# Kernel optimization log

Measured on AMD Instinct MI355X. Metric: run time of the kernel, lower is better.

The kernel has to match this reference:

```python
import jax, jax.numpy as jnp
import numpy as np

N_NODES = 100000
SAMPLES = 16


def setup_inputs() -> dict:
    key = jax.random.key(0)
    ks = jax.random.split(key, 9)
    x = jax.random.normal(ks[0], (N_NODES, 128), dtype=jnp.float32)
    neigh_idx = jax.random.randint(ks[1], (N_NODES, SAMPLES), 0, N_NODES)
    batch = jax.random.randint(ks[2], (8192,), 0, N_NODES)
    W1 = jax.random.normal(ks[3], (256, 128), dtype=jnp.float32) * 0.05
    b1 = jax.random.normal(ks[4], (128,), dtype=jnp.float32) * 0.05
    W2 = jax.random.normal(ks[5], (256, 128), dtype=jnp.float32) * 0.05
    b2 = jax.random.normal(ks[6], (128,), dtype=jnp.float32) * 0.05
    Wout = jax.random.normal(ks[7], (128, 64), dtype=jnp.float32) * 0.05
    bout = jax.random.normal(ks[8], (64,), dtype=jnp.float32) * 0.05
    return {"x": x, "neigh_idx": neigh_idx, "batch": batch,
            "W1": W1, "b1": b1, "W2": W2, "b2": b2,
            "Wout": Wout, "bout": bout}


def _sage_layer(h, neigh_idx, W, b):
    # h: [N, d]; gather sampled neighbors -> [N, S, d]; max-aggregate; concat-linear
    neigh = h[neigh_idx]                     # irregular gather, memory-bound core
    agg = jnp.max(neigh, axis=1)             # MaxAggregation over samples
    feats = jnp.concatenate([h, agg], axis=-1)  # [N, 2d]
    return feats @ W + b


def reference(x, neigh_idx, batch, W1, b1, W2, b2, Wout, bout):
    # layer 1: relu(Linear(concat(x, max_neigh(x))))
    h1 = jax.nn.relu(_sage_layer(x, neigh_idx, W1, b1))
    # layer 2 (== n_layers): Linear output (no relu) fed straight into proj_out
    h2 = _sage_layer(h1, neigh_idx, W2, b2)
    out = h2 @ Wout + bout                   # proj_out (Dropout is eval identity)
    return out[batch]
```

## Files before the change

kernel.cpp:

```cpp
#include <hip/hip_runtime.h>
#include <cmath>
#include <cstdint>

#define N_NODES 100000
#define SAMPLES 16
#define DIM 128
#define NBATCH 8192

#define FSTR 264
#define H2STR 132

typedef _Float16 half8 __attribute__((ext_vector_type(8)));
typedef float floatx4 __attribute__((ext_vector_type(4)));

__device__ __forceinline__ half8 h8max(half8 a, half8 b) {
    half8 r;
#pragma unroll
    for (int i = 0; i < 8; ++i) r[i] = (a[i] > b[i]) ? a[i] : b[i];
    return r;
}

__global__ __launch_bounds__(256) void setup_kernel(
    const float* __restrict__ x,
    const float* __restrict__ W1,
    const float* __restrict__ W2,
    const int* __restrict__ batch,
    const int* __restrict__ nidx,
    int* __restrict__ flags,
    _Float16* __restrict__ xh,
    _Float16* __restrict__ W1sw,
    _Float16* __restrict__ W2sw) {
    const int bid = blockIdx.x;
    if (bid < 6250) {
        const size_t base = ((size_t)bid * 256 + threadIdx.x) * 8;
        const float4* xp = (const float4*)(x + base);
        const float4 a = xp[0], b = xp[1];
        half8 v;
        v[0] = (_Float16)a.x; v[1] = (_Float16)a.y;
        v[2] = (_Float16)a.z; v[3] = (_Float16)a.w;
        v[4] = (_Float16)b.x; v[5] = (_Float16)b.y;
        v[6] = (_Float16)b.z; v[7] = (_Float16)b.w;
        *(half8*)(xh + base) = v;
    } else if (bid < 6282) {
        const int tid = (bid - 6250) * 256 + threadIdx.x;
        const int which = tid >> 12;
        const int r = tid & 4095;
        const int kb = r >> 9, nb = (r >> 6) & 7, lane = r & 63;
        const int q = lane >> 4, c = lane & 15;
        const float* W = which ? W2 : W1;
        _Float16* O = which ? W2sw : W1sw;
        const int k0 = kb * 32 + q * 8;
        const int n = nb * 16 + c;
        half8 v;
#pragma unroll
        for (int j = 0; j < 8; ++j) v[j] = (_Float16)W[(size_t)(k0 + j) * DIM + n];
        *(half8*)(O + (size_t)r * 8) = v;
    } else {
        const int j = (bid - 6282) * 256 + threadIdx.x;
        if (j < NBATCH) {
            const int b = batch[j];
            flags[b] = 1;
            const int* row = nidx + (size_t)b * SAMPLES;
#pragma unroll
            for (int s = 0; s < SAMPLES; ++s) flags[row[s]] = 1;
        }
    }
}

__global__ __launch_bounds__(256, 3) void layer1_kernel(
    const _Float16* __restrict__ xh,
    const int* __restrict__ nidx,
    const _Float16* __restrict__ W1sw,
    const float* __restrict__ b1,
    const int* __restrict__ flags,
    _Float16* __restrict__ h1h) {
    const int wave = threadIdx.x >> 6;
    const int lane = threadIdx.x & 63;
    const int q = lane >> 4;
    const int c = lane & 15;
    const int w0 = blockIdx.x * 64 + wave * 16;

    const int i = w0 + c;
    const bool fi = (i < N_NODES) && (flags[i] == 1);

    half8 sk[4], mk[4];
#pragma unroll
    for (int j = 0; j < 4; ++j)
#pragma unroll
        for (int e = 0; e < 8; ++e) { sk[j][e] = (_Float16)0.f; mk[j][e] = (_Float16)(-60000.f); }

    if (fi) {
        const char* xb = (const char*)xh;
        const int4* ip = (const int4*)(nidx + (size_t)i * SAMPLES);
        const int4 i0 = ip[0], i1 = ip[1], i2 = ip[2], i3 = ip[3];
        const int qb = q * 16;
        const int soff = i * 256 + qb;
        int off[16];
        off[0]  = i0.x * 256 + qb; off[1]  = i0.y * 256 + qb;
        off[2]  = i0.z * 256 + qb; off[3]  = i0.w * 256 + qb;
        off[4]  = i1.x * 256 + qb; off[5]  = i1.y * 256 + qb;
        off[6]  = i1.z * 256 + qb; off[7]  = i1.w * 256 + qb;
        off[8]  = i2.x * 256 + qb; off[9]  = i2.y * 256 + qb;
        off[10] = i2.z * 256 + qb; off[11] = i2.w * 256 + qb;
        off[12] = i3.x * 256 + qb; off[13] = i3.y * 256 + qb;
        off[14] = i3.z * 256 + qb; off[15] = i3.w * 256 + qb;
#pragma unroll
        for (int j = 0; j < 4; ++j) {
            sk[j] = *(const half8*)(xb + soff + j * 64);
            half8 v[16];
#pragma unroll
            for (int s = 0; s < 16; ++s)
                v[s] = *(const half8*)(xb + off[s] + j * 64);
#pragma unroll
            for (int s = 0; s < 8; ++s) v[s] = h8max(v[s], v[s + 8]);
#pragma unroll
            for (int s = 0; s < 4; ++s) v[s] = h8max(v[s], v[s + 4]);
            mk[j] = h8max(h8max(v[0], v[1]), h8max(v[2], v[3]));
        }
    }

    floatx4 acc[8];
#pragma unroll
    for (int nb = 0; nb < 8; ++nb) acc[nb] = (floatx4){0.f, 0.f, 0.f, 0.f};
#pragma unroll
    for (int kb = 0; kb < 8; ++kb) {
        const half8 a = (kb < 4) ? sk[kb] : mk[kb - 4];
#pragma unroll
        for (int nb = 0; nb < 8; ++nb) {
            const half8 b = *(const half8*)(W1sw + (size_t)((kb * 8 + nb) * 64 + lane) * 8);
            acc[nb] = __builtin_amdgcn_mfma_f32_16x16x32_f16(a, b, acc[nb], 0, 0, 0);
        }
    }

#pragma unroll
    for (int r = 0; r < 4; ++r) {
        const int node = w0 + q * 4 + r;
        if (node >= N_NODES || flags[node] != 1) continue;
#pragma unroll
        for (int nb = 0; nb < 8; ++nb) {
            const int n = nb * 16 + c;
            const float v = fmaxf(acc[nb][r] + b1[n], 0.f);
            h1h[(size_t)node * DIM + n] = (_Float16)v;
        }
    }
}

__global__ __launch_bounds__(256) void layer2_kernel(
    const _Float16* __restrict__ h1h,
    const int* __restrict__ nidx,
    const int* __restrict__ batch,
    const _Float16* __restrict__ W2sw,
    const float* __restrict__ b2,
    const float* __restrict__ Wout,
    const float* __restrict__ bout,
    float* __restrict__ out) {
    const int t = threadIdx.x;
    const int wave = t >> 6;
    const int lane = t & 63;
    const int q = lane >> 4, c = lane & 15;
    const int w0 = blockIdx.x * 16;

    __shared__ __align__(16) _Float16 feats[16 * FSTR];
    __shared__ __align__(16) float h2s[16 * H2STR];

    {
        const int m = t >> 4;
        const int cl = t & 15;
        const int node = batch[w0 + m];
        const char* hb = (const char*)h1h;
        const int cb = cl * 16;
        const half8 self = *(const half8*)(hb + node * 256 + cb);
        const int4* ip = (const int4*)(nidx + (size_t)node * SAMPLES);
        const int4 i0 = ip[0], i1 = ip[1], i2 = ip[2], i3 = ip[3];
        int off[16];
        off[0]  = i0.x * 256 + cb; off[1]  = i0.y * 256 + cb;
        off[2]  = i0.z * 256 + cb; off[3]  = i0.w * 256 + cb;
        off[4]  = i1.x * 256 + cb; off[5]  = i1.y * 256 + cb;
        off[6]  = i1.z * 256 + cb; off[7]  = i1.w * 256 + cb;
        off[8]  = i2.x * 256 + cb; off[9]  = i2.y * 256 + cb;
        off[10] = i2.z * 256 + cb; off[11] = i2.w * 256 + cb;
        off[12] = i3.x * 256 + cb; off[13] = i3.y * 256 + cb;
        off[14] = i3.z * 256 + cb; off[15] = i3.w * 256 + cb;
        half8 v[16];
#pragma unroll
        for (int s = 0; s < 16; ++s) v[s] = *(const half8*)(hb + off[s]);
#pragma unroll
        for (int s = 0; s < 8; ++s) v[s] = h8max(v[s], v[s + 8]);
#pragma unroll
        for (int s = 0; s < 4; ++s) v[s] = h8max(v[s], v[s + 4]);
        const half8 mx = h8max(h8max(v[0], v[1]), h8max(v[2], v[3]));
        *(half8*)(feats + m * FSTR + cl * 8) = self;
        *(half8*)(feats + m * FSTR + DIM + cl * 8) = mx;
    }
    __syncthreads();

    const int nb0 = wave * 2;
    floatx4 acc[2];
    acc[0] = (floatx4){0.f, 0.f, 0.f, 0.f};
    acc[1] = (floatx4){0.f, 0.f, 0.f, 0.f};
#pragma unroll
    for (int kb = 0; kb < 8; ++kb) {
        const half8 a = *(const half8*)(feats + c * FSTR + kb * 32 + q * 8);
#pragma unroll
        for (int j = 0; j < 2; ++j) {
            const half8 b = *(const half8*)(W2sw + (size_t)((kb * 8 + nb0 + j) * 64 + lane) * 8);
            acc[j] = __builtin_amdgcn_mfma_f32_16x16x32_f16(a, b, acc[j], 0, 0, 0);
        }
    }
#pragma unroll
    for (int j = 0; j < 2; ++j) {
        const int n = (nb0 + j) * 16 + c;
        const float bias = b2[n];
#pragma unroll
        for (int r = 0; r < 4; ++r)
            h2s[(q * 4 + r) * H2STR + n] = acc[j][r] + bias;
    }
    __syncthreads();

    float accs[4];
    const float bo = bout[lane];
#pragma unroll
    for (int r = 0; r < 4; ++r) accs[r] = bo;
    for (int k4 = 0; k4 < DIM; k4 += 4) {
        float wv[4];
#pragma unroll
        for (int j = 0; j < 4; ++j) wv[j] = Wout[(size_t)(k4 + j) * 64 + lane];
#pragma unroll
        for (int r = 0; r < 4; ++r) {
            const float4 f = *(const float4*)&h2s[(wave * 4 + r) * H2STR + k4];
            accs[r] += f.x * wv[0] + f.y * wv[1] + f.z * wv[2] + f.w * wv[3];
        }
    }
#pragma unroll
    for (int r = 0; r < 4; ++r)
        out[(size_t)(w0 + wave * 4 + r) * 64 + lane] = accs[r];
}

extern "C" void kernel_launch(void* const* d_in, const int* in_sizes, int n_in,
                              void* d_out, int out_size, void* d_ws, size_t ws_size,
                              hipStream_t stream) {
    const float* x    = (const float*)d_in[0];
    const int* nidx   = (const int*)d_in[1];
    const int* batch  = (const int*)d_in[2];
    const float* W1   = (const float*)d_in[3];
    const float* b1   = (const float*)d_in[4];
    const float* W2   = (const float*)d_in[5];
    const float* b2   = (const float*)d_in[6];
    const float* Wout = (const float*)d_in[7];
    const float* bout = (const float*)d_in[8];
    float* out        = (float*)d_out;

    int* flags      = (int*)d_ws;
    _Float16* W1sw  = (_Float16*)((char*)d_ws + 409600);
    _Float16* W2sw  = (_Float16*)((char*)d_ws + 475136);
    _Float16* xh    = (_Float16*)((char*)d_ws + 540672);
    _Float16* h1h   = (_Float16*)((char*)d_ws + 26140672);

    setup_kernel<<<6314, 256, 0, stream>>>(x, W1, W2, batch, nidx, flags, xh, W1sw, W2sw);
    layer1_kernel<<<(N_NODES + 63) / 64, 256, 0, stream>>>(xh, nidx, W1sw, b1, flags, h1h);
    layer2_kernel<<<NBATCH / 16, 256, 0, stream>>>(h1h, nidx, batch, W2sw, b2, Wout, bout, out);
}
```

Baseline: 193.3 us.

## Restructure layer1 to 16 nodes per block with LDS-staged features

Layer1 now handles 16 nodes per block: 16 threads per node each gather one 16-byte chunk from the 16 neighbors, and the self and max features are staged in shared memory. Each wave then computes two of the eight 16-column output tiles with MFMA, reading its A operands from LDS. Per-thread register pressure drops (no eight accumulators and no 4-way unrolled gather), and there are more blocks, so occupancy and memory-level parallelism should rise. The cost is a __syncthreads, extra LDS traffic, and about four times as many blocks, each loading the W1 fragments again.

```diff
diff --git a/kernel.cpp b/kernel.cpp
--- a/kernel.cpp
+++ b/kernel.cpp
@@ -67,79 +67,81 @@
     }
 }
 
-__global__ __launch_bounds__(256, 3) void layer1_kernel(
+__global__ __launch_bounds__(256) void layer1_kernel(
     const _Float16* __restrict__ xh,
     const int* __restrict__ nidx,
     const _Float16* __restrict__ W1sw,
     const float* __restrict__ b1,
     const int* __restrict__ flags,
     _Float16* __restrict__ h1h) {
-    const int wave = threadIdx.x >> 6;
-    const int lane = threadIdx.x & 63;
-    const int q = lane >> 4;
-    const int c = lane & 15;
-    const int w0 = blockIdx.x * 64 + wave * 16;
-
-    const int i = w0 + c;
-    const bool fi = (i < N_NODES) && (flags[i] == 1);
-
-    half8 sk[4], mk[4];
-#pragma unroll
-    for (int j = 0; j < 4; ++j)
-#pragma unroll
-        for (int e = 0; e < 8; ++e) { sk[j][e] = (_Float16)0.f; mk[j][e] = (_Float16)(-60000.f); }
-
+    const int t = threadIdx.x;
+    const int g = t >> 4;
+    const int cl = t & 15;
+    const int i0 = blockIdx.x * 16;
+    const int i = i0 + g;
+
+    __shared__ __align__(16) _Float16 feats[16 * FSTR];
+
+    const bool fi = (flags[i] == 1);
     if (fi) {
         const char* xb = (const char*)xh;
+        const int cb = cl * 16;
+        const half8 self = *(const half8*)(xb + (size_t)i * 256 + cb);
         const int4* ip = (const int4*)(nidx + (size_t)i * SAMPLES);
-        const int4 i0 = ip[0], i1 = ip[1], i2 = ip[2], i3 = ip[3];
-        const int qb = q * 16;
-        const int soff = i * 256 + qb;
+        const int4 a0 = ip[0], a1 = ip[1], a2 = ip[2], a3 = ip[3];
         int off[16];
-        off[0]  = i0.x * 256 + qb; off[1]  = i0.y * 256 + qb;
-        off[2]  = i0.z * 256 + qb; off[3]  = i0.w * 256 + qb;
-        off[4]  = i1.x * 256 + qb; off[5]  = i1.y * 256 + qb;
-        off[6]  = i1.z * 256 + qb; off[7]  = i1.w * 256 + qb;
-        off[8]  = i2.x * 256 + qb; off[9]  = i2.y * 256 + qb;
-        off[10] = i2.z * 256 + qb; off[11] = i2.w * 256 + qb;
-        off[12] = i3.x * 256 + qb; off[13] = i3.y * 256 + qb;
-        off[14] = i3.z * 256 + qb; off[15] = i3.w * 256 + qb;
-#pragma unroll
-        for (int j = 0; j < 4; ++j) {
-            sk[j] = *(const half8*)(xb + soff + j * 64);
-            half8 v[16];
-#pragma unroll
-            for (int s = 0; s < 16; ++s)
-                v[s] = *(const half8*)(xb + off[s] + j * 64);
-#pragma unroll
-            for (int s = 0; s < 8; ++s) v[s] = h8max(v[s], v[s + 8]);
-#pragma unroll
-            for (int s = 0; s < 4; ++s) v[s] = h8max(v[s], v[s + 4]);
-            mk[j] = h8max(h8max(v[0], v[1]), h8max(v[2], v[3]));
-        }
-    }
-
-    floatx4 acc[8];
-#pragma unroll
-    for (int nb = 0; nb < 8; ++nb) acc[nb] = (floatx4){0.f, 0.f, 0.f, 0.f};
+        off[0]  = a0.x * 256 + cb; off[1]  = a0.y * 256 + cb;
+        off[2]  = a0.z * 256 + cb; off[3]  = a0.w * 256 + cb;
+        off[4]  = a1.x * 256 + cb; off[5]  = a1.y * 256 + cb;
+        off[6]  = a1.z * 256 + cb; off[7]  = a1.w * 256 + cb;
+        off[8]  = a2.x * 256 + cb; off[9]  = a2.y * 256 + cb;
+        off[10] = a2.z * 256 + cb; off[11] = a2.w * 256 + cb;
+        off[12] = a3.x * 256 + cb; off[13] = a3.y * 256 + cb;
+        off[14] = a3.z * 256 + cb; off[15] = a3.w * 256 + cb;
+        half8 v[16];
+#pragma unroll
+        for (int s = 0; s < 16; ++s) v[s] = *(const half8*)(xb + off[s]);
+#pragma unroll
+        for (int s = 0; s < 8; ++s) v[s] = h8max(v[s], v[s + 8]);
+#pragma unroll
+        for (int s = 0; s < 4; ++s) v[s] = h8max(v[s], v[s + 4]);
+        const half8 mx = h8max(h8max(v[0], v[1]), h8max(v[2], v[3]));
+        *(half8*)(feats + g * FSTR + cl * 8) = self;
+        *(half8*)(feats + g * FSTR + DIM + cl * 8) = mx;
+    } else {
+        half8 z;
+#pragma unroll
+        for (int e = 0; e < 8; ++e) z[e] = (_Float16)0.f;
+        *(half8*)(feats + g * FSTR + cl * 8) = z;
+        *(half8*)(feats + g * FSTR + DIM + cl * 8) = z;
+    }
+    __syncthreads();
+
+    const int wave = t >> 6;
+    const int lane = t & 63;
+    const int q = lane >> 4, c = lane & 15;
+    const int nb0 = wave * 2;
+    floatx4 acc[2];
+    acc[0] = (floatx4){0.f, 0.f, 0.f, 0.f};
+    acc[1] = (floatx4){0.f, 0.f, 0.f, 0.f};
 #pragma unroll
     for (int kb = 0; kb < 8; ++kb) {
-        const half8 a = (kb < 4) ? sk[kb] : mk[kb - 4];
-#pragma unroll
-        for (int nb = 0; nb < 8; ++nb) {
-            const half8 b = *(const half8*)(W1sw + (size_t)((kb * 8 + nb) * 64 + lane) * 8);
-            acc[nb] = __builtin_amdgcn_mfma_f32_16x16x32_f16(a, b, acc[nb], 0, 0, 0);
+        const half8 a = *(const half8*)(feats + c * FSTR + kb * 32 + q * 8);
+#pragma unroll
+        for (int j = 0; j < 2; ++j) {
+            const half8 b = *(const half8*)(W1sw + (size_t)((kb * 8 + nb0 + j) * 64 + lane) * 8);
+            acc[j] = __builtin_amdgcn_mfma_f32_16x16x32_f16(a, b, acc[j], 0, 0, 0);
         }
     }
 
 #pragma unroll
     for (int r = 0; r < 4; ++r) {
-        const int node = w0 + q * 4 + r;
-        if (node >= N_NODES || flags[node] != 1) continue;
-#pragma unroll
-        for (int nb = 0; nb < 8; ++nb) {
-            const int n = nb * 16 + c;
-            const float v = fmaxf(acc[nb][r] + b1[n], 0.f);
+        const int node = i0 + q * 4 + r;
+        if (flags[node] != 1) continue;
+#pragma unroll
+        for (int j = 0; j < 2; ++j) {
+            const int n = (nb0 + j) * 16 + c;
+            const float v = fmaxf(acc[j][r] + b1[n], 0.f);
             h1h[(size_t)node * DIM + n] = (_Float16)v;
         }
     }
@@ -169,18 +171,18 @@
         const int node = batch[w0 + m];
         const char* hb = (const char*)h1h;
         const int cb = cl * 16;
-        const half8 self = *(const half8*)(hb + node * 256 + cb);
+        const half8 self = *(const half8*)(hb + (size_t)node * 256 + cb);
         const int4* ip = (const int4*)(nidx + (size_t)node * SAMPLES);
-        const int4 i0 = ip[0], i1 = ip[1], i2 = ip[2], i3 = ip[3];
+        const int4 a0 = ip[0], a1 = ip[1], a2 = ip[2], a3 = ip[3];
         int off[16];
-        off[0]  = i0.x * 256 + cb; off[1]  = i0.y * 256 + cb;
-        off[2]  = i0.z * 256 + cb; off[3]  = i0.w * 256 + cb;
-        off[4]  = i1.x * 256 + cb; off[5]  = i1.y * 256 + cb;
-        off[6]  = i1.z * 256 + cb; off[7]  = i1.w * 256 + cb;
-        off[8]  = i2.x * 256 + cb; off[9]  = i2.y * 256 + cb;
-        off[10] = i2.z * 256 + cb; off[11] = i2.w * 256 + cb;
-        off[12] = i3.x * 256 + cb; off[13] = i3.y * 256 + cb;
-        off[14] = i3.z * 256 + cb; off[15] = i3.w * 256 + cb;
+        off[0]  = a0.x * 256 + cb; off[1]  = a0.y * 256 + cb;
+        off[2]  = a0.z * 256 + cb; off[3]  = a0.w * 256 + cb;
+        off[4]  = a1.x * 256 + cb; off[5]  = a1.y * 256 + cb;
+        off[6]  = a1.z * 256 + cb; off[7]  = a1.w * 256 + cb;
+        off[8]  = a2.x * 256 + cb; off[9]  = a2.y * 256 + cb;
+        off[10] = a2.z * 256 + cb; off[11] = a2.w * 256 + cb;
+        off[12] = a3.x * 256 + cb; off[13] = a3.y * 256 + cb;
+        off[14] = a3.z * 256 + cb; off[15] = a3.w * 256 + cb;
         half8 v[16];
 #pragma unroll
         for (int s = 0; s < 16; ++s) v[s] = *(const half8*)(hb + off[s]);
@@ -257,6 +259,6 @@
     _Float16* h1h   = (_Float16*)((char*)d_ws + 26140672);
 
     setup_kernel<<<6314, 256, 0, stream>>>(x, W1, W2, batch, nidx, flags, xh, W1sw, W2sw);
-    layer1_kernel<<<(N_NODES + 63) / 64, 256, 0, stream>>>(xh, nidx, W1sw, b1, flags, h1h);
+    layer1_kernel<<<N_NODES / 16, 256, 0, stream>>>(xh, nidx, W1sw, b1, flags, h1h);
     layer2_kernel<<<NBATCH / 16, 256, 0, stream>>>(h1h, nidx, batch, W2sw, b2, Wout, bout, out);
 }
```

Result: faster. 173.4 us (-10.3%).
